# Kernel optimization log

Hardware: AMD Instinct MI355X
Metric: run time of the kernel (lower is better)

Reference implementation:

```python
import jax, jax.numpy as jnp
import numpy as np

D_MODEL = 2048
N_HEADS = 16
HEAD_DIM = D_MODEL // N_HEADS  # 128
MAX_T = 2048
ROPE_BASE = 10000.0


def _rope_tables(head_dim, max_t, base):
    inv = 1.0 / (base ** (np.arange(0, head_dim, 2, dtype=np.float32) / head_dim))
    t = np.arange(max_t, dtype=np.float32)
    fr = np.outer(t, inv)  # (T, head_dim//2)
    return jnp.asarray(np.cos(fr)), jnp.asarray(np.sin(fr))


def setup_inputs() -> dict:
    key = jax.random.key(0)
    k1, k2, k3 = jax.random.split(key, 3)
    B, T = 2, 2048
    x = jax.random.normal(k1, (B, T, D_MODEL), dtype=jnp.float32)
    Wqkv = jax.random.normal(k2, (3 * D_MODEL, D_MODEL), dtype=jnp.float32) * 0.02
    Wout = jax.random.normal(k3, (D_MODEL, D_MODEL), dtype=jnp.float32) * 0.02
    cos, sin = _rope_tables(HEAD_DIM, MAX_T, ROPE_BASE)
    rope_mask = jnp.arange(N_HEADS) < (N_HEADS // 2)  # first 8 heads RoPE, rest NoPE
    return {"x": x, "Wqkv": Wqkv, "Wout": Wout, "cos": cos, "sin": sin, "rope_mask": rope_mask}


def _apply_rope(t, cos, sin):
    # t: (B,H,T,hd); pairs are consecutive elements (x0,x1),(x2,x3),...
    B, H, T, hd = t.shape
    tr = t.reshape(B, H, T, hd // 2, 2)
    c = cos[:T][None, None, :, :]
    s = sin[:T][None, None, :, :]
    re = tr[..., 0] * c - tr[..., 1] * s
    im = tr[..., 0] * s + tr[..., 1] * c
    return jnp.stack([re, im], axis=-1).reshape(B, H, T, hd)


def reference(x, Wqkv, Wout, cos, sin, rope_mask):
    B, T, D = x.shape
    H = rope_mask.shape[0]
    hd = D // H
    qkv = x @ Wqkv.T  # (B,T,3D)
    q, k, v = jnp.split(qkv, 3, axis=-1)
    def heads(a):
        return a.reshape(B, T, H, hd).transpose(0, 2, 1, 3)  # (B,H,T,hd)
    q, k, v = heads(q), heads(k), heads(v)
    m = rope_mask[None, :, None, None]  # broadcast over (B,H,T,hd)
    q = jnp.where(m, _apply_rope(q, cos, sin), q)
    k = jnp.where(m, _apply_rope(k, cos, sin), k)
    scale = 1.0 / jnp.sqrt(jnp.asarray(hd, dtype=q.dtype))
    scores = jnp.einsum('bhtd,bhsd->bhts', q, k) * scale
    causal = jnp.tril(jnp.ones((T, T), dtype=bool))
    scores = jnp.where(causal[None, None], scores, jnp.asarray(-jnp.inf, dtype=scores.dtype))
    p = jax.nn.softmax(scores, axis=-1)
    out = jnp.einsum('bhts,bhsd->bhtd', p, v)
    out = out.transpose(0, 2, 1, 3).reshape(B, T, D)
    return out @ Wout.T
```

## Files before the change

### kernel.cpp

```cpp
#include <hip/hip_runtime.h>
#include <stdint.h>

typedef unsigned short u16;
typedef __attribute__((ext_vector_type(8))) short short8;
typedef __attribute__((ext_vector_type(4))) short s16x4;
typedef __attribute__((ext_vector_type(4))) float f32x4;
typedef __attribute__((ext_vector_type(16))) float f32x16;

__device__ __forceinline__ u16 f2bf(float f) {
  uint32_t x = __float_as_uint(f);
  x += 0x7fff + ((x >> 16) & 1);
  return (u16)(x >> 16);
}
__device__ __forceinline__ float bf2f(u16 u) {
  return __uint_as_float(((uint32_t)u) << 16);
}
__device__ __forceinline__ f32x4 mfma16(short8 a, short8 b, f32x4 c) {
  return __builtin_amdgcn_mfma_f32_16x16x32_bf16(a, b, c, 0, 0, 0);
}
__device__ __forceinline__ f32x16 mfma32(short8 a, short8 b, f32x16 c) {
  return __builtin_amdgcn_mfma_f32_32x32x16_bf16(a, b, c, 0, 0, 0);
}
__device__ __forceinline__ f32x4 mfma16k16(s16x4 a, s16x4 b, f32x4 c) {
  return __builtin_amdgcn_mfma_f32_16x16x16bf16_1k(a, b, c, 0, 0, 0);
}
__device__ __forceinline__ void gld16(const u16* g, u16* l) {
  __builtin_amdgcn_global_load_lds(
      (const __attribute__((address_space(1))) unsigned int*)g,
      (__attribute__((address_space(3))) unsigned int*)l, 16, 0, 0);
}
__device__ __forceinline__ float exp2a(float x) {
  float r;
  asm("v_exp_f32 %0, %1" : "=v"(r) : "v"(x));
  return r;
}

#define WAIT_VM(n) asm volatile("s_waitcnt vmcnt(" #n ")" ::: "memory")

__global__ __launch_bounds__(256) void cvt_all(const float* __restrict__ x,
                                               const float* __restrict__ wqkv,
                                               const float* __restrict__ wout,
                                               u16* __restrict__ xb,
                                               u16* __restrict__ wqkvb,
                                               u16* __restrict__ woutb) {
  long i = ((long)blockIdx.x * 256 + threadIdx.x) * 8;
  const float* s;
  u16* d;
  long off;
  if (i < 8388608) {
    s = x; d = xb; off = i;
  } else if (i < 20971520) {
    s = wqkv; d = wqkvb; off = i - 8388608;
  } else {
    s = wout; d = woutb; off = i - 20971520;
  }
  f32x4 a = *(const f32x4*)(s + off);
  f32x4 b = *(const f32x4*)(s + off + 4);
  short8 o;
#pragma unroll
  for (int j = 0; j < 4; j++) {
    o[j] = (short)f2bf(a[j]);
    o[j + 4] = (short)f2bf(b[j]);
  }
  *(short8*)(d + off) = o;
}

__global__ __launch_bounds__(512, 2) void gemm_qkv(const u16* __restrict__ A,
                                                   const u16* __restrict__ Bw,
                                                   u16* __restrict__ q3) {
  __shared__ __align__(16) u16 SA[32768];
  __shared__ __align__(16) u16 SB[32768];
  const int id = blockIdx.x;
  const int swz = (id & 7) * 48 + (id >> 3);
  const int by = swz & 15, bx = swz >> 4;
  const int m0 = by * 256, n0 = bx * 256;
  const int t = threadIdx.x, w = t >> 6, lane = t & 63;
  const int quad = lane >> 4, l15 = lane & 15;
  const int wm = w >> 2, wn = w & 3;
  const int rS = t >> 2, pS = t & 3;
  const int cS = (pS - (rS >> 1)) & 3;
  const size_t arow = (size_t)(m0 + rS) * 2048 + cS * 8;
  const size_t brow = (size_t)(n0 + rS) * 2048 + cS * 8;

#define STAGE_A(kt)                                      \
  {                                                      \
    const u16* ga_ = A + arow + (size_t)(kt) * 32;       \
    u16* la_ = SA + ((kt) & 3) * 8192 + t * 8;           \
    gld16(ga_, la_);                                     \
    gld16(ga_ + (size_t)128 * 2048, la_ + 4096);         \
  }
#define STAGE_B(kt)                                      \
  {                                                      \
    const u16* gb_ = Bw + brow + (size_t)(kt) * 32;      \
    u16* lb_ = SB + ((kt) & 3) * 8192 + t * 8;           \
    gld16(gb_, lb_);                                     \
    gld16(gb_ + (size_t)128 * 2048, lb_ + 4096);         \
  }

  f32x4 acc[8][4] = {};
  const int pq = ((quad + (l15 >> 1)) & 3) * 8;

  STAGE_A(0); STAGE_B(0);
  STAGE_A(1); STAGE_B(1);
  STAGE_A(2); STAGE_B(2);
  WAIT_VM(8);
  __builtin_amdgcn_s_barrier();

#pragma unroll 1
  for (int tau = 0; tau < 64; ++tau) {
    const u16* Sa = SA + (tau & 3) * 8192;
    const u16* Sb = SB + (tau & 3) * 8192;
    short8 af[4], bfr[4];
#pragma unroll
    for (int i = 0; i < 4; i++)
      af[i] = *(const short8*)&Sa[(wm * 128 + i * 16 + l15) * 32 + pq];
#pragma unroll
    for (int n = 0; n < 4; n++)
      bfr[n] = *(const short8*)&Sb[(wn * 64 + n * 16 + l15) * 32 + pq];
    if (tau < 61) STAGE_A(tau + 3);
    __builtin_amdgcn_s_barrier();
    __builtin_amdgcn_s_setprio(1);
#pragma unroll
    for (int mi = 0; mi < 4; mi++)
#pragma unroll
      for (int ni = 0; ni < 4; ni++)
        acc[mi][ni] = mfma16(af[mi], bfr[ni], acc[mi][ni]);
    __builtin_amdgcn_s_setprio(0);
    __builtin_amdgcn_s_barrier();
#pragma unroll
    for (int i = 0; i < 4; i++)
      af[i] = *(const short8*)&Sa[(wm * 128 + 64 + i * 16 + l15) * 32 + pq];
    if (tau < 61) STAGE_B(tau + 3);
    __builtin_amdgcn_s_barrier();
    __builtin_amdgcn_s_setprio(1);
#pragma unroll
    for (int mi = 0; mi < 4; mi++)
#pragma unroll
      for (int ni = 0; ni < 4; ni++)
        acc[4 + mi][ni] = mfma16(af[mi], bfr[ni], acc[4 + mi][ni]);
    __builtin_amdgcn_s_setprio(0);
    if (tau < 61) {
      WAIT_VM(8);
    } else if (tau == 61) {
      WAIT_VM(4);
    } else if (tau == 62) {
      WAIT_VM(0);
    }
    __builtin_amdgcn_s_barrier();
  }
#undef STAGE_A
#undef STAGE_B

  const int which = n0 >> 11;
  const int bb = m0 >> 11, tt0 = m0 & 2047;
  if (which == 2) {
    u16* vbase = q3 + 16777216;
#pragma unroll
    for (int ni = 0; ni < 4; ni++) {
      const int gcol = (n0 & 2047) + wn * 64 + ni * 16 + l15;
      const int hh = gcol >> 7, di = gcol & 127;
      u16* vb = vbase + ((size_t)(bb * 16 + hh) * 128 + di) * 2048;
#pragma unroll
      for (int mi = 0; mi < 8; mi++) {
        const int tloc = tt0 + wm * 128 + mi * 16 + quad * 4;
        s16x4 st;
#pragma unroll
        for (int r = 0; r < 4; r++) st[r] = (short)f2bf(acc[mi][ni][r]);
        *(s16x4*)(vb + tloc) = st;
      }
    }
  } else {
    const float sc = (which == 0) ? 0.1275174f : 1.0f;
    u16* base = q3 + (size_t)which * 8388608;
#pragma unroll
    for (int ni = 0; ni < 4; ni++) {
      const int gcol = (n0 & 2047) + wn * 64 + ni * 16 + l15;
      const int hh = gcol >> 7, di = gcol & 127;
      u16* qb = base + ((size_t)(bb * 16 + hh) * 2048) * 128 + di;
#pragma unroll
      for (int mi = 0; mi < 8; mi++) {
        const int tloc = tt0 + wm * 128 + mi * 16 + quad * 4;
#pragma unroll
        for (int r = 0; r < 4; r++)
          qb[(size_t)(tloc + r) * 128] = f2bf(acc[mi][ni][r] * sc);
      }
    }
  }
}

template <int EPI>
__global__ __launch_bounds__(256) void gemm_bt(const u16* __restrict__ A,
                                               const u16* __restrict__ B,
                                               int K, void* __restrict__ Cv, int N) {
  __shared__ __align__(16) u16 SMEM[8448];
  u16* As = SMEM;
  u16* Bs = SMEM + 4096;
  const int m0 = blockIdx.y * 128, n0 = blockIdx.x * 128;
  const int t = threadIdx.x, w = t >> 6, lane = t & 63;
  const int l31 = lane & 31, half = lane >> 5;
  const int rb = (w >> 1) * 64, cb = (w & 1) * 64;
  f32x16 acc[2][2] = {};
  const int rowS = w * 16 + (lane >> 2);
  const int cS = ((lane & 3) - (rowS >> 1)) & 3;
  const u16* ag = A + (size_t)(m0 + rowS) * K + cS * 8;
  const u16* bg = B + (size_t)(n0 + rowS) * K + cS * 8;
  u16* al = As + w * 512 + lane * 8;
  u16* bl = Bs + w * 512 + lane * 8;
  const size_t rowskip = (size_t)64 * K;
  const int p0 = ((0 * 2 + half + (l31 >> 1)) & 3) * 8;
  const int p1 = ((1 * 2 + half + (l31 >> 1)) & 3) * 8;
  for (int k0 = 0; k0 < K; k0 += 32) {
    __syncthreads();
    gld16(ag, al);
    gld16(ag + rowskip, al + 2048);
    gld16(bg, bl);
    gld16(bg + rowskip, bl + 2048);
    ag += 32;
    bg += 32;
    __syncthreads();
    short8 af[2][2], bfr[2][2];
#pragma unroll
    for (int mi = 0; mi < 2; mi++) {
      af[mi][0] = *(const short8*)&As[(rb + mi * 32 + l31) * 32 + p0];
      af[mi][1] = *(const short8*)&As[(rb + mi * 32 + l31) * 32 + p1];
    }
#pragma unroll
    for (int ni = 0; ni < 2; ni++) {
      bfr[ni][0] = *(const short8*)&Bs[(cb + ni * 32 + l31) * 32 + p0];
      bfr[ni][1] = *(const short8*)&Bs[(cb + ni * 32 + l31) * 32 + p1];
    }
#pragma unroll
    for (int kh = 0; kh < 2; kh++)
#pragma unroll
      for (int mi = 0; mi < 2; mi++)
#pragma unroll
        for (int ni = 0; ni < 2; ni++)
          acc[mi][ni] = mfma32(af[mi][kh], bfr[ni][kh], acc[mi][ni]);
  }

  if (EPI == 0) {
    const int which = n0 >> 11;
    const int hh = (n0 & 2047) >> 7;
    const int bb = m0 >> 11, tt0 = m0 & 2047;
    u16* q3 = (u16*)Cv;
    if (which == 2) {
      u16* vbase = q3 + 16777216 + ((size_t)(bb * 16 + hh) * 128) * 2048;
#pragma unroll
      for (int mi = 0; mi < 2; mi++)
#pragma unroll
        for (int ni = 0; ni < 2; ni++) {
          int di = cb + ni * 32 + l31;
          int trow = tt0 + rb + mi * 32 + half * 4;
#pragma unroll
          for (int rg2 = 0; rg2 < 4; rg2++) {
            s16x4 st;
#pragma unroll
            for (int j = 0; j < 4; j++) st[j] = (short)f2bf(acc[mi][ni][rg2 * 4 + j]);
            *(s16x4*)(vbase + (size_t)di * 2048 + trow + rg2 * 8) = st;
          }
        }
    } else {
      const float sc = (which == 0) ? 0.1275174f : 1.0f;
      u16* base = q3 + (size_t)which * 8388608 + ((size_t)(bb * 16 + hh) * 2048) * 128;
#pragma unroll
      for (int mi = 0; mi < 2; mi++)
#pragma unroll
        for (int ni = 0; ni < 2; ni++) {
          int di = cb + ni * 32 + l31;
          int trow = tt0 + rb + mi * 32 + half * 4;
#pragma unroll
          for (int reg = 0; reg < 16; reg++) {
            int tt = trow + (reg & 3) + 8 * (reg >> 2);
            base[(size_t)tt * 128 + di] = f2bf(acc[mi][ni][reg] * sc);
          }
        }
    }
  } else {
    float* Es = (float*)SMEM;
    float* C = (float*)Cv;
#pragma unroll
    for (int r = 0; r < 4; r++) {
      __syncthreads();
      if ((w >> 1) == (r >> 1)) {
        const int mi = r & 1;
#pragma unroll
        for (int ni = 0; ni < 2; ni++) {
          int col = cb + ni * 32 + l31;
#pragma unroll
          for (int reg = 0; reg < 16; reg++) {
            int lrow = (reg & 3) + 8 * (reg >> 2) + half * 4;
            Es[lrow * 132 + col] = acc[mi][ni][reg];
          }
        }
      }
      __syncthreads();
#pragma unroll
      for (int it = 0; it < 4; it++) {
        int idx = it * 256 + t;
        int row = idx >> 5, ch = idx & 31;
        f32x4 vv = *(const f32x4*)&Es[row * 132 + ch * 4];
        *(f32x4*)&C[(size_t)(m0 + r * 32 + row) * N + n0 + ch * 4] = vv;
      }
    }
  }
}

__global__ __launch_bounds__(256) void rope_k(u16* __restrict__ q, u16* __restrict__ k,
                                              const float* __restrict__ cosT,
                                              const float* __restrict__ sinT) {
  int t = threadIdx.x;
  int row = blockIdx.x * 4 + (t >> 6);
  int i = t & 63;
  int b = row >> 14;
  int h = (row >> 11) & 7;
  int tp = row & 2047;
  size_t base = ((size_t)((b * 16 + h) * 2048 + tp)) * 128 + 2 * i;
  float c = cosT[tp * 64 + i], s = sinT[tp * 64 + i];
  {
    uint32_t u = *(uint32_t*)(q + base);
    float x0 = bf2f((u16)(u & 0xffff)), x1 = bf2f((u16)(u >> 16));
    float re = x0 * c - x1 * s, im = x0 * s + x1 * c;
    *(uint32_t*)(q + base) = (uint32_t)f2bf(re) | ((uint32_t)f2bf(im) << 16);
  }
  {
    uint32_t u = *(uint32_t*)(k + base);
    float x0 = bf2f((u16)(u & 0xffff)), x1 = bf2f((u16)(u >> 16));
    float re = x0 * c - x1 * s, im = x0 * s + x1 * c;
    *(uint32_t*)(k + base) = (uint32_t)f2bf(re) | ((uint32_t)f2bf(im) << 16);
  }
}

__global__ __launch_bounds__(256, 2) void attn_k(const u16* __restrict__ qh,
                                                 const u16* __restrict__ kh,
                                                 const u16* __restrict__ vTh,
                                                 u16* __restrict__ attno) {
  __shared__ __align__(16) u16 Ks[8192];
  __shared__ __align__(16) u16 Vt[8192];
  const int i = blockIdx.x;
  const int jj = i & 255, half = i >> 8;
  const int bh = jj >> 3, t8 = jj & 7;
  const int qt = half ? (15 - t8) : t8;
  const int q0 = qt * 128;
  const int t = threadIdx.x, w = t >> 6, lane = t & 63;
  const int quad = lane >> 4, l15 = lane & 15;
  const size_t bhoff = (size_t)bh * 262144;

  short8 qb[2][4];
  {
    const u16* qp = qh + bhoff + (size_t)(q0 + w * 32 + l15) * 128 + quad * 8;
#pragma unroll
    for (int qq = 0; qq < 2; qq++)
#pragma unroll
      for (int ks = 0; ks < 4; ks++)
        qb[qq][ks] = *(const short8*)(qp + qq * 2048 + ks * 32);
  }
  f32x4 of[2][8] = {};
  float mst[2] = {-1e30f, -1e30f}, lst[2] = {0.f, 0.f};
  const int nkt = 2 * qt + 2;
  const int wq0 = q0 + w * 32;

  for (int kt = 0; kt < nkt; kt++) {
    const int k0 = kt * 64;
    __syncthreads();
    {
#pragma unroll
      for (int it = 0; it < 4; it++) {
        int L = it * 256 + t;
        int key = L >> 4, c = L & 15;
        gld16(kh + bhoff + (size_t)(k0 + key) * 128 + ((c ^ (key & 15)) * 8),
              Ks + (size_t)L * 8);
      }
#pragma unroll
      for (int it = 0; it < 4; it++) {
        int L = it * 256 + t;
        int d = L >> 3, c = L & 7;
        gld16(vTh + bhoff + (size_t)d * 2048 + k0 + ((c ^ (d & 7)) * 8),
              Vt + (size_t)L * 8);
      }
    }
    __syncthreads();
    if (k0 <= wq0 + 31) {
      f32x4 sacc[2][4];
#pragma unroll
      for (int qq = 0; qq < 2; qq++)
#pragma unroll
        for (int kk = 0; kk < 4; kk++) sacc[qq][kk] = (f32x4){0.f, 0.f, 0.f, 0.f};
#pragma unroll
      for (int kk = 0; kk < 4; kk++) {
        short8 kf[4];
#pragma unroll
        for (int ks = 0; ks < 4; ks++)
          kf[ks] = *(const short8*)&Ks[(kk * 16 + l15) * 128 + ((ks * 4 + quad) ^ l15) * 8];
#pragma unroll
        for (int qq = 0; qq < 2; qq++)
#pragma unroll
          for (int ks = 0; ks < 4; ks++)
            sacc[qq][kk] = mfma16(kf[ks], qb[qq][ks], sacc[qq][kk]);
      }
      const bool needmask = (k0 + 63 > wq0);
      s16x4 pf[2][4];
      float alpha[2];
#pragma unroll
      for (int qq = 0; qq < 2; qq++) {
        const int qg = wq0 + qq * 16 + l15;
        if (needmask) {
#pragma unroll
          for (int kk = 0; kk < 4; kk++)
#pragma unroll
            for (int rg = 0; rg < 4; rg++)
              if (k0 + kk * 16 + quad * 4 + rg > qg) sacc[qq][kk][rg] = -1e30f;
        }
        float pm = -1e30f;
#pragma unroll
        for (int kk = 0; kk < 4; kk++)
#pragma unroll
          for (int rg = 0; rg < 4; rg++) pm = fmaxf(pm, sacc[qq][kk][rg]);
        pm = fmaxf(pm, __shfl_xor(pm, 16));
        pm = fmaxf(pm, __shfl_xor(pm, 32));
        float mnew = fmaxf(mst[qq], pm);
        alpha[qq] = exp2a(mst[qq] - mnew);
        mst[qq] = mnew;
        float ps = 0.f;
#pragma unroll
        for (int kk = 0; kk < 4; kk++) {
          float e0 = exp2a(sacc[qq][kk][0] - mnew);
          float e1 = exp2a(sacc[qq][kk][1] - mnew);
          float e2 = exp2a(sacc[qq][kk][2] - mnew);
          float e3 = exp2a(sacc[qq][kk][3] - mnew);
          ps += (e0 + e1) + (e2 + e3);
          pf[qq][kk][0] = (short)f2bf(e0);
          pf[qq][kk][1] = (short)f2bf(e1);
          pf[qq][kk][2] = (short)f2bf(e2);
          pf[qq][kk][3] = (short)f2bf(e3);
        }
        ps += __shfl_xor(ps, 16);
        ps += __shfl_xor(ps, 32);
        lst[qq] = lst[qq] * alpha[qq] + ps;
      }
#pragma unroll
      for (int qq = 0; qq < 2; qq++) {
        if (!__all(alpha[qq] == 1.0f)) {
          float a = alpha[qq];
#pragma unroll
          for (int df = 0; df < 8; df++) of[qq][df] *= a;
        }
      }
#pragma unroll
      for (int df = 0; df < 8; df++) {
        s16x4 vf[4];
#pragma unroll
        for (int kk = 0; kk < 4; kk++)
          vf[kk] = *(const s16x4*)&Vt[(df * 16 + l15) * 64 +
                                      ((kk * 2 + (quad >> 1)) ^ (l15 & 7)) * 8 +
                                      (quad & 1) * 4];
#pragma unroll
        for (int qq = 0; qq < 2; qq++)
#pragma unroll
          for (int kk = 0; kk < 4; kk++)
            of[qq][df] = mfma16k16(vf[kk], pf[qq][kk], of[qq][df]);
      }
    }
  }
  const int b = bh >> 4, h = bh & 15;
#pragma unroll
  for (int qq = 0; qq < 2; qq++) {
    float linv = 1.0f / lst[qq];
    const size_t row = (size_t)(b * 2048 + q0 + w * 32 + qq * 16 + l15);
#pragma unroll
    for (int df = 0; df < 8; df++) {
      s16x4 o;
#pragma unroll
      for (int rg = 0; rg < 4; rg++) o[rg] = (short)f2bf(of[qq][df][rg] * linv);
      *(s16x4*)(attno + row * 2048 + h * 128 + df * 16 + quad * 4) = o;
    }
  }
}

extern "C" void kernel_launch(void* const* d_in, const int* in_sizes, int n_in,
                              void* d_out, int out_size, void* d_ws, size_t ws_size,
                              hipStream_t stream) {
  const float* x = (const float*)d_in[0];
  const float* Wqkv = (const float*)d_in[1];
  const float* Wout = (const float*)d_in[2];
  const float* cosT = (const float*)d_in[3];
  const float* sinT = (const float*)d_in[4];
  float* out = (float*)d_out;
  char* ws = (char*)d_ws;
  u16* qkvh = (u16*)(ws + 0);
  u16* woutb = (u16*)(ws + 50331648);
  u16* xb = (u16*)(ws + 58720256);
  u16* wqkvb = (u16*)(ws + 75497472);
  u16* attno = wqkvb;

  cvt_all<<<12288, 256, 0, stream>>>(x, Wqkv, Wout, xb, wqkvb, woutb);
  gemm_qkv<<<384, 512, 0, stream>>>(xb, wqkvb, qkvh);
  rope_k<<<8192, 256, 0, stream>>>(qkvh, qkvh + 8388608, cosT, sinT);
  attn_k<<<512, 256, 0, stream>>>(qkvh, qkvh + 8388608, qkvh + 16777216, attno);
  gemm_bt<1><<<dim3(16, 32), 256, 0, stream>>>(attno, woutb, 2048, (void*)out, 2048);
}
```

Baseline: 408.2 us.

## Unroll QKV GEMM main loop by ring depth and use one barrier per tile

The QKV projection GEMM main loop is unrolled four times so the LDS ring slot is a compile-time constant. Each k-tile now issues the A and B global-to-LDS prefetch together at the start, loads all A and B fragments up front, and runs all 32 MFMAs back to back. It keeps one barrier per tile instead of four. The aim is to cut barrier and scheduling overhead inside the loop; the cost is more live fragment registers (af2), which could hurt occupancy under the 512x2 launch bounds.

```diff
diff --git a/kernel.cpp b/kernel.cpp
--- a/kernel.cpp
+++ b/kernel.cpp
@@ -82,74 +82,64 @@
   const size_t arow = (size_t)(m0 + rS) * 2048 + cS * 8;
   const size_t brow = (size_t)(n0 + rS) * 2048 + cS * 8;
 
-#define STAGE_A(kt)                                      \
-  {                                                      \
-    const u16* ga_ = A + arow + (size_t)(kt) * 32;       \
-    u16* la_ = SA + ((kt) & 3) * 8192 + t * 8;           \
-    gld16(ga_, la_);                                     \
-    gld16(ga_ + (size_t)128 * 2048, la_ + 4096);         \
-  }
-#define STAGE_B(kt)                                      \
-  {                                                      \
-    const u16* gb_ = Bw + brow + (size_t)(kt) * 32;      \
-    u16* lb_ = SB + ((kt) & 3) * 8192 + t * 8;           \
-    gld16(gb_, lb_);                                     \
-    gld16(gb_ + (size_t)128 * 2048, lb_ + 4096);         \
-  }
-
   f32x4 acc[8][4] = {};
   const int pq = ((quad + (l15 >> 1)) & 3) * 8;
 
-  STAGE_A(0); STAGE_B(0);
-  STAGE_A(1); STAGE_B(1);
-  STAGE_A(2); STAGE_B(2);
+#define STAGE_PAIR(KT)                                                        \
+  {                                                                           \
+    const u16* ga_ = A + arow + (size_t)(KT) * 32;                            \
+    u16* la_ = SA + ((KT) & 3) * 8192 + t * 8;                                \
+    gld16(ga_, la_);                                                          \
+    gld16(ga_ + (size_t)128 * 2048, la_ + 4096);                              \
+    const u16* gb_ = Bw + brow + (size_t)(KT) * 32;                           \
+    u16* lb_ = SB + ((KT) & 3) * 8192 + t * 8;                                \
+    gld16(gb_, lb_);                                                          \
+    gld16(gb_ + (size_t)128 * 2048, lb_ + 4096);                              \
+  }
+
+#define TILE(RING, TAU, DO_STAGE, WAIT)                                       \
+  {                                                                           \
+    const u16* Sa_ = SA + (RING) * 8192;                                      \
+    const u16* Sb_ = SB + (RING) * 8192;                                      \
+    if (DO_STAGE) STAGE_PAIR((TAU) + 3);                                      \
+    short8 af[4], af2[4], bfr[4];                                             \
+    _Pragma("unroll") for (int i = 0; i < 4; i++)                             \
+        af[i] = *(const short8*)&Sa_[(wm * 128 + i * 16 + l15) * 32 + pq];    \
+    _Pragma("unroll") for (int n = 0; n < 4; n++)                             \
+        bfr[n] = *(const short8*)&Sb_[(wn * 64 + n * 16 + l15) * 32 + pq];    \
+    _Pragma("unroll") for (int i = 0; i < 4; i++)                             \
+        af2[i] = *(const short8*)&Sa_[(wm * 128 + 64 + i * 16 + l15) * 32 + pq]; \
+    __builtin_amdgcn_s_setprio(1);                                            \
+    _Pragma("unroll") for (int mi = 0; mi < 4; mi++)                          \
+      _Pragma("unroll") for (int ni = 0; ni < 4; ni++)                        \
+          acc[mi][ni] = mfma16(af[mi], bfr[ni], acc[mi][ni]);                 \
+    _Pragma("unroll") for (int mi = 0; mi < 4; mi++)                          \
+      _Pragma("unroll") for (int ni = 0; ni < 4; ni++)                        \
+          acc[4 + mi][ni] = mfma16(af2[mi], bfr[ni], acc[4 + mi][ni]);        \
+    __builtin_amdgcn_s_setprio(0);                                            \
+    WAIT;                                                                     \
+    __builtin_amdgcn_s_barrier();                                             \
+  }
+
+  STAGE_PAIR(0);
+  STAGE_PAIR(1);
+  STAGE_PAIR(2);
   WAIT_VM(8);
   __builtin_amdgcn_s_barrier();
 
 #pragma unroll 1
-  for (int tau = 0; tau < 64; ++tau) {
-    const u16* Sa = SA + (tau & 3) * 8192;
-    const u16* Sb = SB + (tau & 3) * 8192;
-    short8 af[4], bfr[4];
-#pragma unroll
-    for (int i = 0; i < 4; i++)
-      af[i] = *(const short8*)&Sa[(wm * 128 + i * 16 + l15) * 32 + pq];
-#pragma unroll
-    for (int n = 0; n < 4; n++)
-      bfr[n] = *(const short8*)&Sb[(wn * 64 + n * 16 + l15) * 32 + pq];
-    if (tau < 61) STAGE_A(tau + 3);
-    __builtin_amdgcn_s_barrier();
-    __builtin_amdgcn_s_setprio(1);
-#pragma unroll
-    for (int mi = 0; mi < 4; mi++)
-#pragma unroll
-      for (int ni = 0; ni < 4; ni++)
-        acc[mi][ni] = mfma16(af[mi], bfr[ni], acc[mi][ni]);
-    __builtin_amdgcn_s_setprio(0);
-    __builtin_amdgcn_s_barrier();
-#pragma unroll
-    for (int i = 0; i < 4; i++)
-      af[i] = *(const short8*)&Sa[(wm * 128 + 64 + i * 16 + l15) * 32 + pq];
-    if (tau < 61) STAGE_B(tau + 3);
-    __builtin_amdgcn_s_barrier();
-    __builtin_amdgcn_s_setprio(1);
-#pragma unroll
-    for (int mi = 0; mi < 4; mi++)
-#pragma unroll
-      for (int ni = 0; ni < 4; ni++)
-        acc[4 + mi][ni] = mfma16(af[mi], bfr[ni], acc[4 + mi][ni]);
-    __builtin_amdgcn_s_setprio(0);
-    if (tau < 61) {
-      WAIT_VM(8);
-    } else if (tau == 61) {
-      WAIT_VM(4);
-    } else if (tau == 62) {
-      WAIT_VM(0);
-    }
-    __builtin_amdgcn_s_barrier();
-  }
-#undef STAGE_A
-#undef STAGE_B
+  for (int kt = 0; kt < 60; kt += 4) {
+    TILE(0, kt + 0, true, WAIT_VM(8));
+    TILE(1, kt + 1, true, WAIT_VM(8));
+    TILE(2, kt + 2, true, WAIT_VM(8));
+    TILE(3, kt + 3, true, WAIT_VM(8));
+  }
+  TILE(0, 60, true, WAIT_VM(8));
+  TILE(1, 61, false, WAIT_VM(4));
+  TILE(2, 62, false, WAIT_VM(0));
+  TILE(3, 63, false, (void)0);
+#undef TILE
+#undef STAGE_PAIR
 
   const int which = n0 >> 11;
   const int bb = m0 >> 11, tt0 = m0 & 2047;
```

After: 408.8 us. No clear change (+0.1%).
